# Kernel tuning notes

Measured on AMD Instinct MI355X. Metric: run time of the kernel, lower is better.

Reference implementation:

```python
import jax, jax.numpy as jnp
import numpy as np

D_MODEL = 1024
N_HEADS = 16
HEAD_DIM = D_MODEL // N_HEADS
SEQ = 4096
BATCH = 4


def setup_inputs() -> dict:
    key = jax.random.key(0)
    ks = jax.random.split(key, 10)
    s = 0.02
    inp = {
        "h": jax.random.normal(ks[0], (SEQ, BATCH, D_MODEL), jnp.float32),
        "x": jax.random.normal(ks[1], (SEQ, BATCH, D_MODEL), jnp.float32),
        "Wq": jax.random.normal(ks[2], (D_MODEL, D_MODEL), jnp.float32) * s,
        "bq": jnp.zeros((D_MODEL,), jnp.float32),
        "Wk": jax.random.normal(ks[3], (D_MODEL, D_MODEL), jnp.float32) * s,
        "bk": jnp.zeros((D_MODEL,), jnp.float32),
        "Wv": jax.random.normal(ks[4], (D_MODEL, D_MODEL), jnp.float32) * s,
        "bv": jnp.zeros((D_MODEL,), jnp.float32),
        "Wo": jax.random.normal(ks[5], (D_MODEL, D_MODEL), jnp.float32) * s,
        "bo": jnp.zeros((D_MODEL,), jnp.float32),
    }
    return inp


def _heads(t):
    # [S, B, D] -> [B, H, S, d]
    S, B, _ = t.shape
    return t.reshape(S, B, N_HEADS, HEAD_DIM).transpose(1, 2, 0, 3)


def reference(h, x, Wq, bq, Wk, bk, Wv, bv, Wo, bo):
    # torch Linear: y = x @ W.T + b
    Q = _heads(h @ Wq.T + bq)
    K = _heads(x @ Wk.T + bk)
    V = _heads(x @ Wv.T + bv)
    Qp = jax.nn.elu(Q) + 1.0
    Kp = jax.nn.elu(K) + 1.0
    KV = jnp.einsum('bhsd,bhsv->bhdv', Kp, V)          # [B,H,d,d]
    K_sum = Kp.sum(axis=2)                              # [B,H,d]
    Z = jnp.einsum('bhsd,bhd->bhs', Qp, K_sum) + 1e-6   # [B,H,S]
    out = jnp.einsum('bhsd,bhdv->bhsv', Qp, KV) / Z[..., None]
    # [B,H,S,d] -> [S,B,D]
    S, B = h.shape[0], h.shape[1]
    out = out.transpose(2, 0, 1, 3).reshape(S, B, D_MODEL)
    return out @ Wo.T + bo
```

## Files before the change

### kernel.cpp

```cpp
#include <hip/hip_runtime.h>
#include <hip/hip_bf16.h>
#include <cstdint>
#include <cstddef>

#define S_LEN   4096
#define BATCHN  4
#define DMODEL  1024
#define NHEADS  16
#define HDIM    64
#define MROWS   (S_LEN*BATCHN)
#define KDIM    1024
#define NTK     (KDIM/32)
#define CLP     136

typedef __bf16 bf16;
typedef bf16 bf16x8 __attribute__((ext_vector_type(8)));
typedef bf16 bf16x4 __attribute__((ext_vector_type(4)));
typedef float f32x4 __attribute__((ext_vector_type(4)));

#define MFMA16(a,b,c) __builtin_amdgcn_mfma_f32_16x16x32_bf16(a,b,c,0,0,0)

__device__ __forceinline__ void gll16(const void* g, void* l) {
  __builtin_amdgcn_global_load_lds((const __attribute__((address_space(1))) unsigned*)g,
                                   (__attribute__((address_space(3))) unsigned*)l,
                                   16, 0, 0);
}

__global__ __launch_bounds__(256) void cast_all(
    const float* __restrict__ h, const float* __restrict__ x,
    const float* __restrict__ Wq, const float* __restrict__ Wk,
    const float* __restrict__ Wv, const float* __restrict__ Wo,
    bf16* __restrict__ dst) {
  const int nperm = MROWS * KDIM;
  const int ntot  = 2 * nperm + 4 * 1048576;
  int stride = gridDim.x * blockDim.x * 4;
  for (int i = (blockIdx.x * blockDim.x + threadIdx.x) * 4; i < ntot; i += stride) {
    if (i < 2 * nperm) {
      const bool isH = (i < nperm);
      const int j = isH ? i : i - nperm;
      int s = j >> 12, b = (j >> 10) & 3, d = j & 1023;
      size_t o = ((size_t)(b * S_LEN + s) << 10) | d;
      float4 f = *(const float4*)((isH ? h : x) + j);
      bf16x4 u; u[0]=(bf16)f.x; u[1]=(bf16)f.y; u[2]=(bf16)f.z; u[3]=(bf16)f.w;
      *(bf16x4*)(dst + (isH ? 0 : nperm) + o) = u;
    } else {
      int j = i - 2 * nperm;
      int r = j >> 20;
      const float* src = (r < 1) ? (Wq + j) : (r < 2) ? (Wk + j - 1048576)
                       : (r < 3) ? (Wv + j - 2097152) : (Wo + j - 3145728);
      float4 f = *(const float4*)src;
      bf16x4 u; u[0]=(bf16)f.x; u[1]=(bf16)f.y; u[2]=(bf16)f.z; u[3]=(bf16)f.w;
      *(bf16x4*)(dst + i) = u;
    }
  }
}

struct GemmAcc { f32x4 a[4][4]; };

__device__ __forceinline__ void gemm_tile(const bf16* __restrict__ A,
                                          const bf16* __restrict__ Bw,
                                          size_t arow0, size_t brow0,
                                          bf16* sm, GemmAcc& G) {
  const int tid  = threadIdx.x;
  const int wid  = tid >> 6;
  const int lane = tid & 63;
  const int wm = wid >> 1, wn = wid & 1;
  const int lr = lane >> 2;
  const int lc = lane & 3;
  const int ssrc = (((lc << 4) ^ (((lr >> 1) & 3) << 4)) >> 1);
  const int fhalf = (lane >> 4) << 4;

  const bf16* ap[2]; const bf16* bp[2]; int sdo[2];
  #pragma unroll
  for (int i = 0; i < 2; ++i) {
    int seg = (wid << 1) | i;
    ap[i] = A  + (arow0 + seg*16 + lr) * KDIM + ssrc;
    bp[i] = Bw + (brow0 + seg*16 + lr) * KDIM + ssrc;
    sdo[i] = seg * 512;
  }

  #pragma unroll
  for (int i = 0; i < 2; ++i) { gll16(ap[i],      sm + sdo[i]); gll16(bp[i],      sm + 4096 + sdo[i]); }
  #pragma unroll
  for (int i = 0; i < 2; ++i) { gll16(ap[i] + 32, sm + 8192 + sdo[i]); gll16(bp[i] + 32, sm + 12288 + sdo[i]); }
  asm volatile("s_waitcnt vmcnt(4)" ::: "memory");
  __builtin_amdgcn_s_barrier();
  asm volatile("" ::: "memory");

  int cur = 0;
  for (int t = 0; t < NTK; ++t) {
    const bf16* As = sm + cur * 8192;
    const bf16* Bs = As + 4096;

    bf16x8 af[4], bfv[4];
    #pragma unroll
    for (int m = 0; m < 4; ++m) {
      int R = wm*64 + m*16 + (lane & 15);
      af[m] = *(const bf16x8*)((const char*)As + R*64 + (fhalf ^ (((R >> 1) & 3) << 4)));
    }
    #pragma unroll
    for (int n = 0; n < 4; ++n) {
      int R = wn*64 + n*16 + (lane & 15);
      bfv[n] = *(const bf16x8*)((const char*)Bs + R*64 + (fhalf ^ (((R >> 1) & 3) << 4)));
    }

    if (t + 2 < NTK) {
      int nx2 = cur + 2; if (nx2 >= 3) nx2 -= 3;
      bf16* wbA = sm + nx2 * 8192;
      const int ko = (t + 2) * 32;
      #pragma unroll
      for (int i = 0; i < 2; ++i) {
        gll16(ap[i] + ko, wbA + sdo[i]);
        gll16(bp[i] + ko, wbA + 4096 + sdo[i]);
      }
    }

    #pragma unroll
    for (int m = 0; m < 4; ++m)
      #pragma unroll
      for (int n = 0; n < 4; ++n)
        G.a[m][n] = MFMA16(af[m], bfv[n], G.a[m][n]);

    if (t < NTK - 2)       asm volatile("s_waitcnt vmcnt(4)" ::: "memory");
    else if (t == NTK - 2) asm volatile("s_waitcnt vmcnt(0)" ::: "memory");
    if (t < NTK - 1) {
      __builtin_amdgcn_s_barrier();
      asm volatile("" ::: "memory");
    }
    cur = (cur == 2) ? 0 : cur + 1;
  }
}

__global__ __launch_bounds__(256) void q_gemm(
    const bf16* __restrict__ A, const bf16* __restrict__ Bw,
    const float* __restrict__ bq, const float* __restrict__ Ksumg,
    bf16* __restrict__ qs) {
  __shared__ __align__(16) bf16 sm[3 * 8192];
  const int tid  = threadIdx.x;
  const int wid  = tid >> 6;
  const int lane = tid & 63;
  const int wm = wid >> 1, wn = wid & 1;
  const int bid = blockIdx.x;
  const int xcd = bid & 7, local = bid >> 3;
  const int mtile = xcd * 16 + (local >> 3);
  const int ntile = local & 7;

  GemmAcc G = {};
  gemm_tile(A, Bw, (size_t)mtile * 128, (size_t)ntile * 128, sm, G);

  const int hgg = (mtile >> 5) * 16 + ntile * 2 + wn;
  float ksl[4], bql[4];
  #pragma unroll
  for (int n = 0; n < 4; ++n) {
    ksl[n] = Ksumg[hgg*64 + n*16 + (lane & 15)];
    bql[n] = bq[ntile*128 + wn*64 + n*16 + (lane & 15)];
  }

  #pragma unroll
  for (int m = 0; m < 4; ++m) {
    #pragma unroll
    for (int i = 0; i < 4; ++i) {
      int row = mtile*128 + wm*64 + m*16 + ((lane >> 4) << 2) + i;
      float v[4], zp = 0.f;
      #pragma unroll
      for (int n = 0; n < 4; ++n) {
        float t = G.a[m][n][i] + bql[n];
        t = (t > 0.f) ? t + 1.f : __expf(t);
        v[n] = t;
        zp += t * ksl[n];
      }
      zp += __shfl_xor(zp, 1);
      zp += __shfl_xor(zp, 2);
      zp += __shfl_xor(zp, 4);
      zp += __shfl_xor(zp, 8);
      float rz = 1.f / (zp + 1e-6f);
      #pragma unroll
      for (int n = 0; n < 4; ++n) {
        int col = ntile*128 + wn*64 + n*16 + (lane & 15);
        qs[(size_t)row*DMODEL + col] = (bf16)(v[n] * rz);
      }
    }
  }
}

__global__ __launch_bounds__(256) void out_gemm(const bf16* __restrict__ qsA,
                                                const bf16* __restrict__ B2,
                                                const float* __restrict__ bo,
                                                float* __restrict__ Cout) {
  __shared__ __align__(16) bf16 sm[3 * 8192];
  const int tid  = threadIdx.x;
  const int wid  = tid >> 6;
  const int lane = tid & 63;
  const int wm = wid >> 1, wn = wid & 1;
  const int bid = blockIdx.x;
  const int xcd = bid & 7, local = bid >> 3;
  const int mtile = xcd * 16 + (local >> 3);
  const int ntile = local & 7;
  const bf16* Bw = B2 + (size_t)(mtile >> 5) * 1048576;

  GemmAcc G = {};
  gemm_tile(qsA, Bw, (size_t)mtile * 128, (size_t)ntile * 128, sm, G);

  #pragma unroll
  for (int m = 0; m < 4; ++m) {
    int rowb = mtile*128 + wm*64 + m*16 + ((lane >> 4) << 2);
    #pragma unroll
    for (int n = 0; n < 4; ++n) {
      int col = ntile*128 + wn*64 + n*16 + (lane & 15);
      float bias = bo[col];
      #pragma unroll
      for (int i = 0; i < 4; ++i) {
        int g = rowb + i;
        int orow = ((g & 4095) << 2) | (g >> 12);
        Cout[(size_t)orow*DMODEL + col] = G.a[m][n][i] + bias;
      }
    }
  }
}

__global__ __launch_bounds__(512, 4) void kvproj(
    const bf16* __restrict__ Wkv, const bf16* __restrict__ xb,
    const float* __restrict__ bk, const float* __restrict__ bv,
    float* __restrict__ kvb, float* __restrict__ ksb) {
  __shared__ __align__(16) bf16 sm[3 * 12288];
  const int tid  = threadIdx.x;
  const int wid  = tid >> 6;
  const int lane = tid & 63;
  const int wm = wid >> 1, wn = wid & 1;
  const int bid = blockIdx.x;
  const int xcd = bid & 7, local = bid >> 3;
  const int ntile = xcd * 16 + (local >> 3);
  const int m = local & 7;
  const int lr = lane >> 2;
  const int lc = lane & 3;
  const int ssrc = (((lc << 4) ^ (((lr >> 1) & 3) << 4)) >> 1);
  const int fhalf = (lane >> 4) << 4;

  const bf16* KA = Wkv + (size_t)(m * 128) * KDIM;
  const bf16* VA = Wkv + (size_t)(1024 + m * 128) * KDIM;
  const bf16* BB = xb + (size_t)(ntile * 128) * KDIM;

  const bf16* ap[2]; const bf16* bp; int sda[2], sdb;
  #pragma unroll
  for (int i = 0; i < 2; ++i) {
    int seg = (wid << 1) | i;
    const bf16* base = (seg < 8) ? KA : VA;
    ap[i] = base + (size_t)((seg & 7) * 16 + lr) * KDIM + ssrc;
    sda[i] = seg * 512;
  }
  bp = BB + (size_t)(wid * 16 + lr) * KDIM + ssrc;
  sdb = 8192 + wid * 512;

  #pragma unroll
  for (int i = 0; i < 2; ++i) gll16(ap[i], sm + sda[i]);
  gll16(bp, sm + sdb);
  #pragma unroll
  for (int i = 0; i < 2; ++i) gll16(ap[i] + 32, sm + 12288 + sda[i]);
  gll16(bp + 32, sm + 12288 + sdb);
  asm volatile("s_waitcnt vmcnt(3)" ::: "memory");
  __builtin_amdgcn_s_barrier();
  asm volatile("" ::: "memory");

  f32x4 acc[4][4] = {};
  int cur = 0;
  for (int t = 0; t < NTK; ++t) {
    const bf16* As = sm + cur * 12288;
    const bf16* Bs = As + 8192;

    bf16x8 af[4], bfv[4];
    #pragma unroll
    for (int mm = 0; mm < 4; ++mm) {
      int R = wm*64 + mm*16 + (lane & 15);
      af[mm] = *(const bf16x8*)((const char*)As + R*64 + (fhalf ^ (((R >> 1) & 3) << 4)));
    }
    #pragma unroll
    for (int nn = 0; nn < 4; ++nn) {
      int R = wn*64 + nn*16 + (lane & 15);
      bfv[nn] = *(const bf16x8*)((const char*)Bs + R*64 + (fhalf ^ (((R >> 1) & 3) << 4)));
    }

    if (t + 2 < NTK) {
      int nx2 = cur + 2; if (nx2 >= 3) nx2 -= 3;
      bf16* wb = sm + nx2 * 12288;
      const int ko = (t + 2) * 32;
      #pragma unroll
      for (int i = 0; i < 2; ++i) gll16(ap[i] + ko, wb + sda[i]);
      gll16(bp + ko, wb + sdb);
    }

    #pragma unroll
    for (int mm = 0; mm < 4; ++mm)
      #pragma unroll
      for (int nn = 0; nn < 4; ++nn)
        acc[mm][nn] = MFMA16(af[mm], bfv[nn], acc[mm][nn]);

    if (t < NTK - 2)       asm volatile("s_waitcnt vmcnt(3)" ::: "memory");
    else if (t == NTK - 2) asm volatile("s_waitcnt vmcnt(0)" ::: "memory");
    if (t < NTK - 1) {
      __builtin_amdgcn_s_barrier();
      asm volatile("" ::: "memory");
    }
    cur = (cur == 2) ? 0 : cur + 1;
  }
  __syncthreads();

  bf16* CL = sm;
  #pragma unroll
  for (int mm = 0; mm < 4; ++mm) {
    #pragma unroll
    for (int i = 0; i < 4; ++i) {
      int ra = wm*64 + mm*16 + ((lane >> 4) << 2) + i;
      float bias = (ra < 128) ? bk[m*128 + ra] : bv[m*128 + ra - 128];
      #pragma unroll
      for (int nn = 0; nn < 4; ++nn) {
        int cb = wn*64 + nn*16 + (lane & 15);
        float v = acc[mm][nn][i] + bias;
        if (ra < 128) v = (v > 0.f) ? v + 1.f : __expf(v);
        CL[ra*CLP + cb] = (bf16)v;
      }
    }
  }
  __syncthreads();

  const int hl = wid >> 2;
  const int ww = wid & 3;
  const int bh = (ntile >> 5) * 16 + 2*m + hl;
  f32x4 acc2[4] = {};
  #pragma unroll
  for (int ks = 0; ks < 4; ++ks) {
    bf16x8 akv = *(const bf16x8*)(CL + (hl*64 + ww*16 + (lane & 15))*CLP + ks*32 + ((lane >> 4) << 3));
    #pragma unroll
    for (int nn = 0; nn < 4; ++nn) {
      bf16x8 bkv = *(const bf16x8*)(CL + (128 + hl*64 + nn*16 + (lane & 15))*CLP + ks*32 + ((lane >> 4) << 3));
      acc2[nn] = MFMA16(akv, bkv, acc2[nn]);
    }
  }
  float* KVh = kvb + (size_t)bh * 4096;
  #pragma unroll
  for (int nn = 0; nn < 4; ++nn)
    #pragma unroll
    for (int i = 0; i < 4; ++i) {
      int dd = ww*16 + ((lane >> 4) << 2) + i;
      int vv = nn*16 + (lane & 15);
      atomicAdd(&KVh[dd*64 + vv], acc2[nn][i]);
    }

  {
    int rid = tid >> 2, part = tid & 3;
    float s = 0.f;
    #pragma unroll
    for (int j = 0; j < 32; ++j) s += (float)CL[rid*CLP + part*32 + j];
    s += __shfl_xor(s, 1);
    s += __shfl_xor(s, 2);
    if (part == 0) {
      int hh = rid >> 6, d = rid & 63;
      atomicAdd(&ksb[((ntile >> 5) * 16 + 2*m + hh)*64 + d], s);
    }
  }
}

__global__ __launch_bounds__(256) void w2_gemm(const bf16* __restrict__ wob,
                                               const float* __restrict__ kvb,
                                               bf16* __restrict__ B2) {
  const int mtile = blockIdx.x, bh = blockIdx.y;
  const int b = bh >> 4, hh = bh & 15;
  const int tid = threadIdx.x;
  const int wid = tid >> 6, lane = tid & 63;
  __shared__ __align__(16) bf16 Wos[128*64];
  __shared__ __align__(16) bf16 KVs[64*64];

  #pragma unroll
  for (int it = 0; it < 4; ++it) {
    int idx = it*256 + tid;
    int row = idx >> 3, c = (idx & 7) << 3;
    *(bf16x8*)(Wos + row*64 + c) =
      *(const bf16x8*)(wob + (size_t)(mtile*128 + row)*DMODEL + hh*64 + c);
  }
  const float* KVh = kvb + (size_t)bh * 4096;
  #pragma unroll
  for (int it = 0; it < 16; ++it) {
    int idx = it*256 + tid;
    KVs[idx] = (bf16)KVh[idx];
  }
  __syncthreads();

  f32x4 acc[2][4] = {};
  #pragma unroll
  for (int ks = 0; ks < 2; ++ks) {
    bf16x8 af[2], bv[4];
    #pragma unroll
    for (int m = 0; m < 2; ++m)
      af[m] = *(const bf16x8*)(Wos + (wid*32 + m*16 + (lane & 15))*64 + ks*32 + ((lane>>4)<<3));
    #pragma unroll
    for (int n = 0; n < 4; ++n)
      bv[n] = *(const bf16x8*)(KVs + (n*16 + (lane & 15))*64 + ks*32 + ((lane>>4)<<3));
    #pragma unroll
    for (int m = 0; m < 2; ++m)
      #pragma unroll
      for (int n = 0; n < 4; ++n)
        acc[m][n] = MFMA16(af[m], bv[n], acc[m][n]);
  }

  bf16* B2b = B2 + (size_t)b * 1048576;
  #pragma unroll
  for (int m = 0; m < 2; ++m)
    #pragma unroll
    for (int n = 0; n < 4; ++n)
      #pragma unroll
      for (int i = 0; i < 4; ++i) {
        int orow = mtile*128 + wid*32 + m*16 + ((lane >> 4) << 2) + i;
        int dd   = n*16 + (lane & 15);
        B2b[(size_t)orow*DMODEL + hh*64 + dd] = (bf16)acc[m][n][i];
      }
}

extern "C" void kernel_launch(void* const* d_in, const int* in_sizes, int n_in,
                              void* d_out, int out_size, void* d_ws, size_t ws_size,
                              hipStream_t stream) {
  const float* h  = (const float*)d_in[0];
  const float* x  = (const float*)d_in[1];
  const float* Wq = (const float*)d_in[2];
  const float* bq = (const float*)d_in[3];
  const float* Wk = (const float*)d_in[4];
  const float* bk = (const float*)d_in[5];
  const float* Wv = (const float*)d_in[6];
  const float* bv = (const float*)d_in[7];
  const float* Wo = (const float*)d_in[8];
  const float* bo = (const float*)d_in[9];

  char* ws = (char*)d_ws;
  bf16*  hb   = (bf16*)(ws);
  bf16*  xb   = (bf16*)(ws + 33554432);
  bf16*  wcat = (bf16*)(ws + 67108864);
  bf16*  wob  = (bf16*)(ws + 73400320);
  bf16*  qs   = (bf16*)(ws + 75497472);
  float* kvb  = (float*)(ws + 109051904);
  float* ksb  = (float*)(ws + 110100480);
  bf16*  B2   = (bf16*)(ws + 110116864);

  cast_all<<<dim3(4096), 256, 0, stream>>>(h, x, Wq, Wk, Wv, Wo, hb);

  hipMemsetAsync(kvb, 0, 1048576 + 16384, stream);

  kvproj<<<dim3(1024), 512, 0, stream>>>(wcat + 1048576, xb, bk, bv, kvb, ksb);
  w2_gemm<<<dim3(8, 64), 256, 0, stream>>>(wob, kvb, B2);
  q_gemm<<<dim3(1024), 256, 0, stream>>>(hb, wcat, bq, ksb, qs);
  out_gemm<<<dim3(1024), 256, 0, stream>>>(qs, B2, bo, (float*)d_out);
}
```

Measured before the change: 230.5 us.

## Enlarge Q and output GEMM tiles to 256x128 with 8x4 MFMA per wave

The shared GEMM tile routine now computes 256x128 output tiles instead of 128x128. Each wave holds 8x4 accumulators, and the loader is restructured so each wave issues six global-to-LDS loads per K step. Grids are halved to 512 blocks and tile indexing is remapped. The aim is higher arithmetic intensity and less B-operand refetch per output, at the cost of more registers, more LDS (occupancy bound set to 2) and fewer blocks to balance across CUs.

```diff
diff --git a/kernel.cpp b/kernel.cpp
--- a/kernel.cpp
+++ b/kernel.cpp
@@ -55,7 +55,7 @@
   }
 }
 
-struct GemmAcc { f32x4 a[4][4]; };
+struct GemmAcc { f32x4 a[8][4]; };
 
 __device__ __forceinline__ void gemm_tile(const bf16* __restrict__ A,
                                           const bf16* __restrict__ Bw,
@@ -65,63 +65,60 @@
   const int wid  = tid >> 6;
   const int lane = tid & 63;
   const int wm = wid >> 1, wn = wid & 1;
-  const int lr = lane >> 2;
-  const int lc = lane & 3;
-  const int ssrc = (((lc << 4) ^ (((lr >> 1) & 3) << 4)) >> 1);
   const int fhalf = (lane >> 4) << 4;
 
-  const bf16* ap[2]; const bf16* bp[2]; int sdo[2];
-  #pragma unroll
-  for (int i = 0; i < 2; ++i) {
-    int seg = (wid << 1) | i;
-    ap[i] = A  + (arow0 + seg*16 + lr) * KDIM + ssrc;
-    bp[i] = Bw + (brow0 + seg*16 + lr) * KDIM + ssrc;
-    sdo[i] = seg * 512;
-  }
-
-  #pragma unroll
-  for (int i = 0; i < 2; ++i) { gll16(ap[i],      sm + sdo[i]); gll16(bp[i],      sm + 4096 + sdo[i]); }
-  #pragma unroll
-  for (int i = 0; i < 2; ++i) { gll16(ap[i] + 32, sm + 8192 + sdo[i]); gll16(bp[i] + 32, sm + 12288 + sdo[i]); }
-  asm volatile("s_waitcnt vmcnt(4)" ::: "memory");
+  const bf16* sp[6]; int sd[6];
+  #pragma unroll
+  for (int j = 0; j < 6; ++j) {
+    int c = wid * 6 + j;
+    int row; const bf16* src; int dstE;
+    if (c < 16) { row = c * 16 + (lane >> 2); src = A  + (arow0 + row) * KDIM; dstE = c * 512; }
+    else { int cb = c - 16; row = cb * 16 + (lane >> 2); src = Bw + (brow0 + row) * KDIM; dstE = 8192 + cb * 512; }
+    int c16 = lane & 3;
+    sp[j] = src + ((c16 ^ ((row >> 1) & 3)) * 8);
+    sd[j] = dstE;
+  }
+
+  #pragma unroll
+  for (int j = 0; j < 6; ++j) gll16(sp[j],      sm + sd[j]);
+  #pragma unroll
+  for (int j = 0; j < 6; ++j) gll16(sp[j] + 32, sm + 12288 + sd[j]);
+  asm volatile("s_waitcnt vmcnt(6)" ::: "memory");
   __builtin_amdgcn_s_barrier();
   asm volatile("" ::: "memory");
 
   int cur = 0;
   for (int t = 0; t < NTK; ++t) {
-    const bf16* As = sm + cur * 8192;
-    const bf16* Bs = As + 4096;
-
-    bf16x8 af[4], bfv[4];
-    #pragma unroll
-    for (int m = 0; m < 4; ++m) {
-      int R = wm*64 + m*16 + (lane & 15);
-      af[m] = *(const bf16x8*)((const char*)As + R*64 + (fhalf ^ (((R >> 1) & 3) << 4)));
+    const char* As = (const char*)(sm + cur * 12288);
+    const char* Bs = As + 16384;
+
+    bf16x8 af[8], bfv[4];
+    #pragma unroll
+    for (int m = 0; m < 8; ++m) {
+      int R = wm*128 + m*16 + (lane & 15);
+      af[m] = *(const bf16x8*)(As + R*64 + (fhalf ^ (((R >> 1) & 3) << 4)));
     }
     #pragma unroll
     for (int n = 0; n < 4; ++n) {
       int R = wn*64 + n*16 + (lane & 15);
-      bfv[n] = *(const bf16x8*)((const char*)Bs + R*64 + (fhalf ^ (((R >> 1) & 3) << 4)));
+      bfv[n] = *(const bf16x8*)(Bs + R*64 + (fhalf ^ (((R >> 1) & 3) << 4)));
     }
 
     if (t + 2 < NTK) {
       int nx2 = cur + 2; if (nx2 >= 3) nx2 -= 3;
-      bf16* wbA = sm + nx2 * 8192;
+      bf16* wb = sm + nx2 * 12288;
       const int ko = (t + 2) * 32;
       #pragma unroll
-      for (int i = 0; i < 2; ++i) {
-        gll16(ap[i] + ko, wbA + sdo[i]);
-        gll16(bp[i] + ko, wbA + 4096 + sdo[i]);
-      }
-    }
-
-    #pragma unroll
-    for (int m = 0; m < 4; ++m)
+      for (int j = 0; j < 6; ++j) gll16(sp[j] + ko, wb + sd[j]);
+    }
+
+    #pragma unroll
+    for (int m = 0; m < 8; ++m)
       #pragma unroll
       for (int n = 0; n < 4; ++n)
         G.a[m][n] = MFMA16(af[m], bfv[n], G.a[m][n]);
 
-    if (t < NTK - 2)       asm volatile("s_waitcnt vmcnt(4)" ::: "memory");
+    if (t < NTK - 2)       asm volatile("s_waitcnt vmcnt(6)" ::: "memory");
     else if (t == NTK - 2) asm volatile("s_waitcnt vmcnt(0)" ::: "memory");
     if (t < NTK - 1) {
       __builtin_amdgcn_s_barrier();
@@ -131,24 +128,24 @@
   }
 }
 
-__global__ __launch_bounds__(256) void q_gemm(
+__global__ __launch_bounds__(256, 2) void q_gemm(
     const bf16* __restrict__ A, const bf16* __restrict__ Bw,
     const float* __restrict__ bq, const float* __restrict__ Ksumg,
     bf16* __restrict__ qs) {
-  __shared__ __align__(16) bf16 sm[3 * 8192];
+  __shared__ __align__(16) bf16 sm[3 * 12288];
   const int tid  = threadIdx.x;
   const int wid  = tid >> 6;
   const int lane = tid & 63;
   const int wm = wid >> 1, wn = wid & 1;
   const int bid = blockIdx.x;
   const int xcd = bid & 7, local = bid >> 3;
-  const int mtile = xcd * 16 + (local >> 3);
+  const int mtile = xcd * 8 + (local >> 3);
   const int ntile = local & 7;
 
   GemmAcc G = {};
-  gemm_tile(A, Bw, (size_t)mtile * 128, (size_t)ntile * 128, sm, G);
-
-  const int hgg = (mtile >> 5) * 16 + ntile * 2 + wn;
+  gemm_tile(A, Bw, (size_t)mtile * 256, (size_t)ntile * 128, sm, G);
+
+  const int hgg = (mtile >> 4) * 16 + ntile * 2 + wn;
   float ksl[4], bql[4];
   #pragma unroll
   for (int n = 0; n < 4; ++n) {
@@ -157,10 +154,10 @@
   }
 
   #pragma unroll
-  for (int m = 0; m < 4; ++m) {
+  for (int m = 0; m < 8; ++m) {
     #pragma unroll
     for (int i = 0; i < 4; ++i) {
-      int row = mtile*128 + wm*64 + m*16 + ((lane >> 4) << 2) + i;
+      int row = mtile*256 + wm*128 + m*16 + ((lane >> 4) << 2) + i;
       float v[4], zp = 0.f;
       #pragma unroll
       for (int n = 0; n < 4; ++n) {
@@ -183,34 +180,33 @@
   }
 }
 
-__global__ __launch_bounds__(256) void out_gemm(const bf16* __restrict__ qsA,
-                                                const bf16* __restrict__ B2,
-                                                const float* __restrict__ bo,
-                                                float* __restrict__ Cout) {
-  __shared__ __align__(16) bf16 sm[3 * 8192];
+__global__ __launch_bounds__(256, 2) void out_gemm(const bf16* __restrict__ qsA,
+                                                   const bf16* __restrict__ B2,
+                                                   const float* __restrict__ bo,
+                                                   float* __restrict__ Cout) {
+  __shared__ __align__(16) bf16 sm[3 * 12288];
   const int tid  = threadIdx.x;
   const int wid  = tid >> 6;
   const int lane = tid & 63;
   const int wm = wid >> 1, wn = wid & 1;
   const int bid = blockIdx.x;
   const int xcd = bid & 7, local = bid >> 3;
-  const int mtile = xcd * 16 + (local >> 3);
+  const int mtile = xcd * 8 + (local >> 3);
   const int ntile = local & 7;
-  const bf16* Bw = B2 + (size_t)(mtile >> 5) * 1048576;
+  const bf16* Bw = B2 + (size_t)(mtile >> 4) * 1048576;
 
   GemmAcc G = {};
-  gemm_tile(qsA, Bw, (size_t)mtile * 128, (size_t)ntile * 128, sm, G);
-
-  #pragma unroll
-  for (int m = 0; m < 4; ++m) {
-    int rowb = mtile*128 + wm*64 + m*16 + ((lane >> 4) << 2);
+  gemm_tile(qsA, Bw, (size_t)mtile * 256, (size_t)ntile * 128, sm, G);
+
+  #pragma unroll
+  for (int m = 0; m < 8; ++m) {
     #pragma unroll
     for (int n = 0; n < 4; ++n) {
       int col = ntile*128 + wn*64 + n*16 + (lane & 15);
       float bias = bo[col];
       #pragma unroll
       for (int i = 0; i < 4; ++i) {
-        int g = rowb + i;
+        int g = mtile*256 + wm*128 + m*16 + ((lane >> 4) << 2) + i;
         int orow = ((g & 4095) << 2) | (g >> 12);
         Cout[(size_t)orow*DMODEL + col] = G.a[m][n][i] + bias;
       }
@@ -444,6 +440,6 @@
 
   kvproj<<<dim3(1024), 512, 0, stream>>>(wcat + 1048576, xb, bk, bv, kvb, ksb);
   w2_gemm<<<dim3(8, 64), 256, 0, stream>>>(wob, kvb, B2);
-  q_gemm<<<dim3(1024), 256, 0, stream>>>(hb, wcat, bq, ksb, qs);
-  out_gemm<<<dim3(1024), 256, 0, stream>>>(qs, B2, bo, (float*)d_out);
-}
+  q_gemm<<<dim3(512), 256, 0, stream>>>(hb, wcat, bq, ksb, qs);
+  out_gemm<<<dim3(512), 256, 0, stream>>>(qs, B2, bo, (float*)d_out);
+}
```

Result: faster. 221.7 us (median of 2 runs) (-3.8%).
